# Kernel optimization log

Hardware: AMD Instinct MI355X
Metric: run time of the kernel (lower is better)

The kernel has to match this reference:

```python
import jax, jax.numpy as jnp
import numpy as np

N = 100000
E = 1600000
IN, HID, OUT = 128, 256, 128


def setup_inputs() -> dict:
    key = jax.random.key(0)
    ks = jax.random.split(key, 8)
    x = jax.random.normal(ks[0], (N, IN), dtype=jnp.float32)
    edge_index = jax.random.randint(ks[1], (2, E), 0, N, dtype=jnp.int64)
    # PyG SAGEConv params: lin_l (neighbor aggr, with bias), lin_r (root, no bias)
    def glorot(k, shape):
        fan_in = shape[1]
        return jax.random.normal(k, shape, dtype=jnp.float32) / jnp.sqrt(jnp.float32(fan_in))
    W1l = glorot(ks[2], (HID, IN)); b1 = jnp.zeros((HID,), jnp.float32)
    W1r = glorot(ks[3], (HID, IN))
    W2l = glorot(ks[4], (OUT, HID)); b2 = jnp.zeros((OUT,), jnp.float32)
    W2r = glorot(ks[5], (OUT, HID))
    return {"x": x, "edge_index": edge_index, "W1l": W1l, "b1": b1,
            "W1r": W1r, "W2l": W2l, "b2": b2, "W2r": W2r}


def sage_conv(x, row, col, Wl, b, Wr, n_nodes):
    # mean-aggregate neighbor features x[row] at target nodes col
    msg = x[row]                                               # [E, d]
    s = jax.ops.segment_sum(msg, col, num_segments=n_nodes)    # [N, d]
    deg = jax.ops.segment_sum(jnp.ones((row.shape[0], 1), x.dtype), col,
                              num_segments=n_nodes)            # [N, 1]
    mean = s / jnp.maximum(deg, 1.0)
    return mean @ Wl.T + b + x @ Wr.T


def reference(x, edge_index, W1l, b1, W1r, W2l, b2, W2r):
    row, col = edge_index[0], edge_index[1]
    h = sage_conv(x, row, col, W1l, b1, W1r, N)
    h = jax.nn.relu(h)
    # dropout is identity in eval mode
    out = sage_conv(h, row, col, W2l, b2, W2r, N)
    return out
```

## Files before the change

### kernel.cpp

```cpp
#include <hip/hip_runtime.h>
#include <hip/hip_bf16.h>
#include <hip/hip_fp16.h>

#define NN 100000
#define NE 1600000
#define NCHUNK ((NN + 127) / 128)
#define NPB 512
#define NB 256
#define CHUNK 8192
#define NCH ((NE + CHUNK - 1) / CHUNK)

typedef __attribute__((ext_vector_type(8))) short short8;
typedef __attribute__((ext_vector_type(4))) float float4v;
typedef __attribute__((ext_vector_type(2))) float float2v;

__device__ __forceinline__ unsigned short f2bf(float f) {
    unsigned int b = __float_as_uint(f);
    return (unsigned short)((b + 0x7fffu + ((b >> 16) & 1u)) >> 16);
}
__device__ __forceinline__ unsigned int pack_bf16(float lo, float hi) {
    return (unsigned int)f2bf(lo) | ((unsigned int)f2bf(hi) << 16);
}
__device__ __forceinline__ void addp8(float* a, uint2 u) {
    float2v f;
    f = __builtin_amdgcn_cvt_pk_f32_fp8(u.x, false); a[0] += f.x; a[1] += f.y;
    f = __builtin_amdgcn_cvt_pk_f32_fp8(u.x, true);  a[2] += f.x; a[3] += f.y;
    f = __builtin_amdgcn_cvt_pk_f32_fp8(u.y, false); a[4] += f.x; a[5] += f.y;
    f = __builtin_amdgcn_cvt_pk_f32_fp8(u.y, true);  a[6] += f.x; a[7] += f.y;
}
__device__ __forceinline__ unsigned char f2fp8(float v) {
    int r = __builtin_amdgcn_cvt_pk_fp8_f32(v, v, 0, false);
    return (unsigned char)(r & 0xff);
}
__device__ __forceinline__ unsigned short pack2fp8(float lo, float hi) {
    int r = __builtin_amdgcn_cvt_pk_fp8_f32(lo, hi, 0, false);
    return (unsigned short)(r & 0xffff);
}
__device__ __forceinline__ float h2f(unsigned short u) {
    return __half2float(__ushort_as_half(u));
}

__global__ void k_prep(const float* x, const float* W1l, const float* W1r,
                       const float* W2l, const float* W2r, const int* ei,
                       unsigned int* axb_u, unsigned short* xf8, unsigned short* wb1,
                       unsigned short* wb2, int* bcnt) {
    __shared__ int hh[NB];
    int b = blockIdx.x, t = threadIdx.x;
    if (b < 3125) {
#pragma unroll
        for (int k = 0; k < 8; k++) {
            int tt = b * 2048 + k * 256 + t;
            int node = tt >> 6, i = tt & 63;
            float2 v = ((const float2*)x)[tt];
            axb_u[(size_t)node * 128 + 64 + i] = pack_bf16(v.x, v.y);
            xf8[(size_t)node * 64 + i] = pack2fp8(v.x, v.y);
        }
    } else if (b < 3253) {
        int i = (b - 3125) * 256 + t;
        int r1 = i >> 7, c1 = i & 127;
        wb1[r1 * 256 + c1]       = f2bf(W1l[i]);
        wb1[r1 * 256 + 128 + c1] = f2bf(W1r[i]);
        wb2[i]         = f2bf(W2l[i]);
        wb2[32768 + i] = f2bf(W2r[i]);
    } else {
        hh[t] = 0;
        __syncthreads();
        int e0 = (b - 3253) * 6250;
        for (int e = e0 + t; e < e0 + 6250; e += 256)
            atomicAdd(&hh[ei[NE + e] >> 9], 1);
        __syncthreads();
        if (hh[t]) atomicAdd(&bcnt[t], hh[t]);
    }
}

__global__ void k_bscan(const int* bcnt, int* boff, int* bcur) {
    __shared__ int s[NB];
    int t = threadIdx.x;
    int v = bcnt[t];
    s[t] = v;
    __syncthreads();
    for (int d = 1; d < NB; d <<= 1) {
        int val = (t >= d) ? s[t - d] : 0;
        __syncthreads();
        s[t] += val;
        __syncthreads();
    }
    boff[t + 1] = s[t];
    if (t == 0) boff[0] = 0;
    bcur[t] = s[t] - v;
}

__global__ __launch_bounds__(256) void k_bscatter(const int* ei, int* bcur, unsigned int* pairs) {
    __shared__ unsigned int buf[CHUNK];
    __shared__ int cnt[NB];
    __shared__ int lbase[NB];
    __shared__ int lcur[NB];
    __shared__ int gpos[NB];
    int t = threadIdx.x;
    int e0 = blockIdx.x * CHUNK;
    int nedge = NE - e0; if (nedge > CHUNK) nedge = CHUNK;
    cnt[t] = 0;
    __syncthreads();
    for (int i = t; i < nedge; i += 256)
        atomicAdd(&cnt[ei[NE + e0 + i] >> 9], 1);
    __syncthreads();
    int v = cnt[t];
    lcur[t] = v;
    __syncthreads();
    for (int d = 1; d < NB; d <<= 1) {
        int val = (t >= d) ? lcur[t - d] : 0;
        __syncthreads();
        lcur[t] += val;
        __syncthreads();
    }
    lbase[t] = lcur[t] - v;
    gpos[t] = atomicAdd(&bcur[t], v);
    __syncthreads();
    lcur[t] = lbase[t];
    __syncthreads();
    for (int i = t; i < nedge; i += 256) {
        int r = ei[e0 + i], c = ei[NE + e0 + i];
        int b = c >> 9;
        int p = atomicAdd(&lcur[b], 1);
        buf[p] = (unsigned)r | ((unsigned)(c & 511) << 17);
    }
    __syncthreads();
    int wv = t >> 6, lane = t & 63;
    for (int b = wv; b < NB; b += 4) {
        int n = cnt[b], lb = lbase[b], gp = gpos[b];
        for (int i = lane; i < n; i += 64)
            pairs[gp + i] = buf[lb + i];
    }
}

__global__ __launch_bounds__(256) void k_build(const unsigned int* pairs, const int* boff,
                                               int* off, int* deg, int* csr, int* csr16) {
    __shared__ int ldeg[NPB];
    __shared__ int lcur[NPB];
    __shared__ int lini[NPB];
    __shared__ int sscan[256];
    int b = blockIdx.x;
    int nbase = b * NPB;
    if (nbase >= NN) return;
    int t = threadIdx.x;
    int base = boff[b], cntb = boff[b + 1] - base;
    ldeg[t] = 0; ldeg[t + 256] = 0;
    __syncthreads();
    for (int i = t; i < cntb; i += 256) {
        unsigned int pr = pairs[base + i];
        atomicAdd(&ldeg[pr >> 17], 1);
    }
    __syncthreads();
    int d0 = ldeg[2 * t], d1 = ldeg[2 * t + 1];
    int v = d0 + d1;
    sscan[t] = v;
    __syncthreads();
    for (int d = 1; d < 256; d <<= 1) {
        int val = (t >= d) ? sscan[t - d] : 0;
        __syncthreads();
        sscan[t] += val;
        __syncthreads();
    }
    int ex = sscan[t] - v;
    lcur[2 * t] = ex;      lcur[2 * t + 1] = ex + d0;
    lini[2 * t] = ex;      lini[2 * t + 1] = ex + d0;
    __syncthreads();
    int nloc = NN - nbase; if (nloc > NPB) nloc = NPB;
    for (int ln = t; ln < nloc; ln += 256) {
        off[nbase + ln] = base + lcur[ln];
        deg[nbase + ln] = ldeg[ln];
    }
    __syncthreads();
    if (csr16) {
        for (int i = t; i < cntb; i += 256) {
            unsigned int pr = pairs[base + i];
            int nd = pr >> 17;
            int p = atomicAdd(&lcur[nd], 1);
            int src = (int)(pr & 0x1FFFFu);
            csr[base + p] = src;
            int rk = p - lini[nd];
            if (rk < 16) csr16[(size_t)(nbase + nd) * 16 + rk] = src;
        }
    } else {
        for (int i = t; i < cntb; i += 256) {
            unsigned int pr = pairs[base + i];
            int p = atomicAdd(&lcur[pr >> 17], 1);
            csr[base + p] = (int)(pr & 0x1FFFFu);
        }
    }
}

__global__ __launch_bounds__(512) void k_agg1(const uint2* xf8, const int* off, const int* deg,
                                              const int* csr, const int* csr16,
                                              unsigned int* axb_w) {
    int wid = (blockIdx.x * 512 + threadIdx.x) >> 6;
    if (wid >= NN) return;
    int lane = threadIdx.x & 63;
    int sub = lane >> 4, l16 = lane & 15;
    int start = off[wid], d = deg[wid];
    const uint2* gp = xf8 + l16;
    uint2 z; z.x = 0u; z.y = 0u;
    float a[8] = {0.f, 0.f, 0.f, 0.f, 0.f, 0.f, 0.f, 0.f};
    int j;
    if (csr16) {
        int e16 = csr16[(size_t)wid * 16 + l16];
#pragma unroll
        for (int r = 0; r < 4; r++) {
            int rk = (r << 2) | sub;
            int idx = __shfl(e16, rk, 64);
            uint2 u = (rk < d) ? gp[(size_t)idx * 16] : z;
            addp8(a, u);
        }
        j = 16 + sub;
    } else {
        j = sub;
    }
    for (; j + 4 < d; j += 8) {
        int n0 = csr[start + j];
        int n1 = csr[start + j + 4];
        uint2 u0 = gp[(size_t)n0 * 16];
        uint2 u1 = gp[(size_t)n1 * 16];
        addp8(a, u0); addp8(a, u1);
    }
    if (j < d) {
        int nb = csr[start + j];
        uint2 u = gp[(size_t)nb * 16];
        addp8(a, u);
    }
#pragma unroll
    for (int i = 0; i < 8; i++) {
        a[i] += __shfl_xor(a[i], 16, 64);
        a[i] += __shfl_xor(a[i], 32, 64);
    }
    if (sub == 0) {
        float inv = 1.0f / (float)(d > 0 ? d : 1);
        uint4 o;
        o.x = pack_bf16(a[0] * inv, a[1] * inv);
        o.y = pack_bf16(a[2] * inv, a[3] * inv);
        o.z = pack_bf16(a[4] * inv, a[5] * inv);
        o.w = pack_bf16(a[6] * inv, a[7] * inv);
        *(uint4*)(axb_w + (size_t)wid * 128 + (l16 << 2)) = o;
    }
}

__global__ __launch_bounds__(512) void k_agg2(const uint2* g, const int* off, const int* deg,
                                              const int* csr, const int* csr16,
                                              const unsigned short* partial, float* out) {
    int wid = (blockIdx.x * 512 + threadIdx.x) >> 6;
    if (wid >= NN) return;
    int lane = threadIdx.x & 63;
    int sub = lane >> 4, l16 = lane & 15;
    int start = off[wid], d = deg[wid];
    const uint2* gp = g + l16;
    uint2 z; z.x = 0u; z.y = 0u;
    uint4 pu;
    if (sub == 0)
        pu = *(const uint4*)(partial + (size_t)wid * 128 + (l16 << 3));
    float a[8] = {0.f, 0.f, 0.f, 0.f, 0.f, 0.f, 0.f, 0.f};
    int j;
    if (csr16) {
        int e16 = csr16[(size_t)wid * 16 + l16];
#pragma unroll
        for (int r = 0; r < 4; r++) {
            int rk = (r << 2) | sub;
            int idx = __shfl(e16, rk, 64);
            uint2 u = (rk < d) ? gp[(size_t)idx * 16] : z;
            addp8(a, u);
        }
        j = 16 + sub;
    } else {
        j = sub;
    }
    for (; j + 4 < d; j += 8) {
        int n0 = csr[start + j];
        int n1 = csr[start + j + 4];
        uint2 u0 = gp[(size_t)n0 * 16];
        uint2 u1 = gp[(size_t)n1 * 16];
        addp8(a, u0); addp8(a, u1);
    }
    if (j < d) {
        int nb = csr[start + j];
        uint2 u = gp[(size_t)nb * 16];
        addp8(a, u);
    }
#pragma unroll
    for (int i = 0; i < 8; i++) {
        a[i] += __shfl_xor(a[i], 16, 64);
        a[i] += __shfl_xor(a[i], 32, 64);
    }
    if (sub == 0) {
        float inv = 1.0f / (float)(d > 0 ? d : 1);
        float4 c0, c1;
        c0.x = h2f(pu.x & 0xffff) + a[0] * inv; c0.y = h2f(pu.x >> 16) + a[1] * inv;
        c0.z = h2f(pu.y & 0xffff) + a[2] * inv; c0.w = h2f(pu.y >> 16) + a[3] * inv;
        c1.x = h2f(pu.z & 0xffff) + a[4] * inv; c1.y = h2f(pu.z >> 16) + a[5] * inv;
        c1.z = h2f(pu.w & 0xffff) + a[6] * inv; c1.w = h2f(pu.w >> 16) + a[7] * inv;
        float4* po = (float4*)(out + (size_t)wid * 128) + (l16 << 1);
        po[0] = c0; po[1] = c1;
    }
}

#define BROW 264
#define GGRID (32 * ((NCHUNK + 7) / 8))
__global__ __launch_bounds__(256, 4) void k_gemm1(const unsigned short* A, const unsigned short* wb,
                                                  const float* b1, unsigned short* H) {
    __shared__ unsigned short Bs[64 * BROW];
    int t = threadIdx.x;
    int b = blockIdx.x;
    int chunk = (b & 7) + ((b >> 5) << 3);
    int cg = (b >> 3) & 3;
    if (chunk >= NCHUNK) return;
    {
        const short8* src = (const short8*)(wb + (size_t)cg * 64 * 256);
        short8* dst = (short8*)Bs;
#pragma unroll
        for (int i = 0; i < 8; i++) {
            int gi = i * 256 + t;
            int r = gi >> 5, c = gi & 31;
            dst[r * 33 + c] = src[gi];
        }
    }
    __syncthreads();
    int wv = t >> 6, lane = t & 63;
    int mrow = lane & 15, quad = lane >> 4;
    int base = chunk * 128 + wv * 32;
    if (base >= NN) return;
    float bias[4];
#pragma unroll
    for (int ctl = 0; ctl < 4; ctl++) bias[ctl] = b1[cg * 64 + ctl * 16 + mrow];
    float4v acc[2][4];
#pragma unroll
    for (int h = 0; h < 2; h++)
#pragma unroll
        for (int ctl = 0; ctl < 4; ctl++) acc[h][ctl] = (float4v)(0.0f);
    const short8* a0p = (const short8*)(A + (size_t)(base + mrow) * 256);
    const short8* a1p = (const short8*)(A + (size_t)(base + 16 + mrow) * 256);
#pragma unroll
    for (int kk = 0; kk < 8; kk++) {
        short8 a0 = a0p[kk * 4 + quad];
        short8 a1 = a1p[kk * 4 + quad];
        int koff = kk * 32 + quad * 8;
#pragma unroll
        for (int ctl = 0; ctl < 4; ctl++) {
            short8 bfr = *(const short8*)(Bs + (ctl * 16 + mrow) * BROW + koff);
            acc[0][ctl] = __builtin_amdgcn_mfma_f32_16x16x32_bf16(a0, bfr, acc[0][ctl], 0, 0, 0);
            acc[1][ctl] = __builtin_amdgcn_mfma_f32_16x16x32_bf16(a1, bfr, acc[1][ctl], 0, 0, 0);
        }
    }
#pragma unroll
    for (int ctl = 0; ctl < 4; ctl++) {
        int col = cg * 64 + ctl * 16 + mrow;
#pragma unroll
        for (int h = 0; h < 2; h++)
#pragma unroll
            for (int r = 0; r < 4; r++) {
                int node = base + h * 16 + quad * 4 + r;
                float v = acc[h][ctl][r] + bias[ctl];
                H[(size_t)node * 256 + col] = f2bf(fmaxf(v, 0.f));
            }
    }
}

__global__ __launch_bounds__(256, 4) void k_gemm2(const unsigned short* A, const unsigned short* wb,
                                                  const float* b2, unsigned char* g,
                                                  unsigned short* partial) {
    __shared__ unsigned short Bs[64 * BROW];
    int t = threadIdx.x;
    int b = blockIdx.x;
    int chunk = (b & 7) + ((b >> 5) << 3);
    int cg = (b >> 3) & 3;
    if (chunk >= NCHUNK) return;
    {
        const short8* src = (const short8*)(wb + (size_t)cg * 64 * 256);
        short8* dst = (short8*)Bs;
#pragma unroll
        for (int i = 0; i < 8; i++) {
            int gi = i * 256 + t;
            int r = gi >> 5, c = gi & 31;
            dst[r * 33 + c] = src[gi];
        }
    }
    __syncthreads();
    int wv = t >> 6, lane = t & 63;
    int mrow = lane & 15, quad = lane >> 4;
    int base = chunk * 128 + wv * 32;
    if (base >= NN) return;
    float bias[4];
#pragma unroll
    for (int ctl = 0; ctl < 4; ctl++)
        bias[ctl] = (cg >= 2) ? b2[cg * 64 + ctl * 16 + mrow - 128] : 0.f;
    float4v acc[2][4];
#pragma unroll
    for (int h = 0; h < 2; h++)
#pragma unroll
        for (int ctl = 0; ctl < 4; ctl++) acc[h][ctl] = (float4v)(0.0f);
    const short8* a0p = (const short8*)(A + (size_t)(base + mrow) * 256);
    const short8* a1p = (const short8*)(A + (size_t)(base + 16 + mrow) * 256);
#pragma unroll
    for (int kk = 0; kk < 8; kk++) {
        short8 a0 = a0p[kk * 4 + quad];
        short8 a1 = a1p[kk * 4 + quad];
        int koff = kk * 32 + quad * 8;
#pragma unroll
        for (int ctl = 0; ctl < 4; ctl++) {
            short8 bfr = *(const short8*)(Bs + (ctl * 16 + mrow) * BROW + koff);
            acc[0][ctl] = __builtin_amdgcn_mfma_f32_16x16x32_bf16(a0, bfr, acc[0][ctl], 0, 0, 0);
            acc[1][ctl] = __builtin_amdgcn_mfma_f32_16x16x32_bf16(a1, bfr, acc[1][ctl], 0, 0, 0);
        }
    }
    if (cg < 2) {
#pragma unroll
        for (int ctl = 0; ctl < 4; ctl++) {
            int col = cg * 64 + ctl * 16 + mrow;
#pragma unroll
            for (int h = 0; h < 2; h++)
#pragma unroll
                for (int r = 0; r < 4; r++) {
                    int node = base + h * 16 + quad * 4 + r;
                    g[(size_t)node * 128 + col] = f2fp8(acc[h][ctl][r]);
                }
        }
    } else {
#pragma unroll
        for (int ctl = 0; ctl < 4; ctl++) {
            int pcol = cg * 64 + ctl * 16 + mrow - 128;
#pragma unroll
            for (int h = 0; h < 2; h++)
#pragma unroll
                for (int r = 0; r < 4; r++) {
                    int node = base + h * 16 + quad * 4 + r;
                    __half hf = __float2half(acc[h][ctl][r] + bias[ctl]);
                    partial[(size_t)node * 128 + pcol] = __half_as_ushort(hf);
                }
        }
    }
}

extern "C" void kernel_launch(void* const* d_in, const int* in_sizes, int n_in,
                              void* d_out, int out_size, void* d_ws, size_t ws_size,
                              hipStream_t stream) {
    const float* x   = (const float*)d_in[0];
    const int*   ei  = (const int*)d_in[1];
    const float* W1l = (const float*)d_in[2];
    const float* b1  = (const float*)d_in[3];
    const float* W1r = (const float*)d_in[4];
    const float* W2l = (const float*)d_in[5];
    const float* b2  = (const float*)d_in[6];
    const float* W2r = (const float*)d_in[7];
    float* out = (float*)d_out;

    char* p = (char*)d_ws;
    unsigned int* axb = (unsigned int*)p; p += (size_t)NN * 256 * 2;
    unsigned short* h = (unsigned short*)p; p += (size_t)NN * 256 * 2;
    unsigned char* g  = (unsigned char*)p; p += (size_t)NN * 128;
    unsigned short* xf8 = (unsigned short*)p; p += (size_t)NN * 128;
    unsigned short* wb1 = (unsigned short*)p; p += 65536 * 2;
    unsigned short* wb2 = (unsigned short*)p; p += 65536 * 2;
    int* deg  = (int*)p; p += (size_t)NN * 4;
    int* off  = (int*)p; p += (size_t)NN * 4;
    int* csr  = (int*)p; p += (size_t)NE * 4;
    int* bcnt = (int*)p; p += NB * 4;
    int* boff = (int*)p; p += (NB + 1) * 4;
    int* bcur = (int*)p; p += NB * 4;
    if (ws_size < (size_t)(p - (char*)d_ws)) return;
    int* csr16 = (int*)p; p += (size_t)NN * 16 * 4;
    if (ws_size < (size_t)(p - (char*)d_ws)) csr16 = nullptr;
    unsigned int* pairs = (unsigned int*)h;
    unsigned short* partial = (unsigned short*)axb;

    hipMemsetAsync(bcnt, 0, NB * 4, stream);
    k_prep<<<3509, 256, 0, stream>>>(x, W1l, W1r, W2l, W2r, ei, axb, xf8, wb1, wb2, bcnt);
    k_bscan<<<1, NB, 0, stream>>>(bcnt, boff, bcur);
    k_bscatter<<<NCH, 256, 0, stream>>>(ei, bcur, pairs);
    k_build<<<NB, 256, 0, stream>>>(pairs, boff, off, deg, csr, csr16);
    k_agg1<<<12500, 512, 0, stream>>>((const uint2*)xf8, off, deg, csr, csr16, axb);
    k_gemm1<<<GGRID, 256, 0, stream>>>((const unsigned short*)axb, wb1, b1, h);
    k_gemm2<<<GGRID, 256, 0, stream>>>(h, wb2, b2, g, partial);
    k_agg2<<<12500, 512, 0, stream>>>((const uint2*)g, off, deg, csr, csr16, partial, out);
}
```

Before: 356.1 us.

## Restructure aggregation to full-wave per-neighbor gathers with 32-slot padded CSR and zero row

Both aggregation kernels now have each lane own two features, and the whole wave walks neighbors one at a time. This replaces the 4-way sub-wave split and its cross-lane shuffle reduction. The padded per-node neighbor table grows from 16 to 32 slots, and the first 32 neighbors are gathered in a fully unrolled loop. Padding slots point at a zeroed sentinel row N, which k_prep now writes in an extra block, so the loop needs no per-load predicate. This trades 2-byte loads per lane and wasted loads for low-degree nodes (mean degree 16) against more memory-level parallelism and no reduction; the padded table also doubles in size.

```diff
diff --git a/kernel.cpp b/kernel.cpp
--- a/kernel.cpp
+++ b/kernel.cpp
@@ -21,13 +21,6 @@
 __device__ __forceinline__ unsigned int pack_bf16(float lo, float hi) {
     return (unsigned int)f2bf(lo) | ((unsigned int)f2bf(hi) << 16);
 }
-__device__ __forceinline__ void addp8(float* a, uint2 u) {
-    float2v f;
-    f = __builtin_amdgcn_cvt_pk_f32_fp8(u.x, false); a[0] += f.x; a[1] += f.y;
-    f = __builtin_amdgcn_cvt_pk_f32_fp8(u.x, true);  a[2] += f.x; a[3] += f.y;
-    f = __builtin_amdgcn_cvt_pk_f32_fp8(u.y, false); a[4] += f.x; a[5] += f.y;
-    f = __builtin_amdgcn_cvt_pk_f32_fp8(u.y, true);  a[6] += f.x; a[7] += f.y;
-}
 __device__ __forceinline__ unsigned char f2fp8(float v) {
     int r = __builtin_amdgcn_cvt_pk_fp8_f32(v, v, 0, false);
     return (unsigned char)(r & 0xff);
@@ -43,7 +36,7 @@
 __global__ void k_prep(const float* x, const float* W1l, const float* W1r,
                        const float* W2l, const float* W2r, const int* ei,
                        unsigned int* axb_u, unsigned short* xf8, unsigned short* wb1,
-                       unsigned short* wb2, int* bcnt) {
+                       unsigned short* wb2, int* bcnt, unsigned short* gz) {
     __shared__ int hh[NB];
     int b = blockIdx.x, t = threadIdx.x;
     if (b < 3125) {
@@ -62,7 +55,7 @@
         wb1[r1 * 256 + 128 + c1] = f2bf(W1r[i]);
         wb2[i]         = f2bf(W2l[i]);
         wb2[32768 + i] = f2bf(W2r[i]);
-    } else {
+    } else if (b < 3509) {
         hh[t] = 0;
         __syncthreads();
         int e0 = (b - 3253) * 6250;
@@ -70,6 +63,9 @@
             atomicAdd(&hh[ei[NE + e] >> 9], 1);
         __syncthreads();
         if (hh[t]) atomicAdd(&bcnt[t], hh[t]);
+    } else {
+        if (t < 64) xf8[(size_t)NN * 64 + t] = 0;
+        else if (t < 128 && gz) gz[(size_t)NN * 64 + (t - 64)] = 0;
     }
 }
 
@@ -134,7 +130,7 @@
 }
 
 __global__ __launch_bounds__(256) void k_build(const unsigned int* pairs, const int* boff,
-                                               int* off, int* deg, int* csr, int* csr16) {
+                                               int* off, int* deg, int* csr, int* csr32) {
     __shared__ int ldeg[NPB];
     __shared__ int lcur[NPB];
     __shared__ int lini[NPB];
@@ -171,7 +167,7 @@
         deg[nbase + ln] = ldeg[ln];
     }
     __syncthreads();
-    if (csr16) {
+    if (csr32) {
         for (int i = t; i < cntb; i += 256) {
             unsigned int pr = pairs[base + i];
             int nd = pr >> 17;
@@ -179,7 +175,7 @@
             int src = (int)(pr & 0x1FFFFu);
             csr[base + p] = src;
             int rk = p - lini[nd];
-            if (rk < 16) csr16[(size_t)(nbase + nd) * 16 + rk] = src;
+            if (rk < 32) csr32[(size_t)(nbase + nd) * 32 + rk] = src;
         }
     } else {
         for (int i = t; i < cntb; i += 256) {
@@ -190,114 +186,90 @@
     }
 }
 
-__global__ __launch_bounds__(512) void k_agg1(const uint2* xf8, const int* off, const int* deg,
-                                              const int* csr, const int* csr16,
+__global__ __launch_bounds__(512) void k_agg1(const unsigned short* xf8, const int* off,
+                                              const int* deg, const int* csr, const int* csr32,
                                               unsigned int* axb_w) {
     int wid = (blockIdx.x * 512 + threadIdx.x) >> 6;
     if (wid >= NN) return;
+    int widu = __builtin_amdgcn_readfirstlane(wid);
     int lane = threadIdx.x & 63;
-    int sub = lane >> 4, l16 = lane & 15;
-    int start = off[wid], d = deg[wid];
-    const uint2* gp = xf8 + l16;
-    uint2 z; z.x = 0u; z.y = 0u;
-    float a[8] = {0.f, 0.f, 0.f, 0.f, 0.f, 0.f, 0.f, 0.f};
-    int j;
-    if (csr16) {
-        int e16 = csr16[(size_t)wid * 16 + l16];
-#pragma unroll
-        for (int r = 0; r < 4; r++) {
-            int rk = (r << 2) | sub;
-            int idx = __shfl(e16, rk, 64);
-            uint2 u = (rk < d) ? gp[(size_t)idx * 16] : z;
-            addp8(a, u);
-        }
-        j = 16 + sub;
+    int d = deg[widu];
+    float a0 = 0.f, a1 = 0.f;
+    if (csr32) {
+        const int* c32 = csr32 + (size_t)widu * 32;
+        int dm = d < 32 ? d : 32;
+#pragma unroll
+        for (int r = 0; r < 32; r++) {
+            int idx = (r < dm) ? c32[r] : NN;
+            unsigned short u = xf8[(size_t)idx * 64 + lane];
+            float2v f = __builtin_amdgcn_cvt_pk_f32_fp8((unsigned int)u, false);
+            a0 += f.x; a1 += f.y;
+        }
+        if (d > 32) {
+            int start = off[widu];
+            for (int j = 32; j < d; j++) {
+                int idx = csr[start + j];
+                unsigned short u = xf8[(size_t)idx * 64 + lane];
+                float2v f = __builtin_amdgcn_cvt_pk_f32_fp8((unsigned int)u, false);
+                a0 += f.x; a1 += f.y;
+            }
+        }
     } else {
-        j = sub;
-    }
-    for (; j + 4 < d; j += 8) {
-        int n0 = csr[start + j];
-        int n1 = csr[start + j + 4];
-        uint2 u0 = gp[(size_t)n0 * 16];
-        uint2 u1 = gp[(size_t)n1 * 16];
-        addp8(a, u0); addp8(a, u1);
-    }
-    if (j < d) {
-        int nb = csr[start + j];
-        uint2 u = gp[(size_t)nb * 16];
-        addp8(a, u);
-    }
-#pragma unroll
-    for (int i = 0; i < 8; i++) {
-        a[i] += __shfl_xor(a[i], 16, 64);
-        a[i] += __shfl_xor(a[i], 32, 64);
-    }
-    if (sub == 0) {
-        float inv = 1.0f / (float)(d > 0 ? d : 1);
-        uint4 o;
-        o.x = pack_bf16(a[0] * inv, a[1] * inv);
-        o.y = pack_bf16(a[2] * inv, a[3] * inv);
-        o.z = pack_bf16(a[4] * inv, a[5] * inv);
-        o.w = pack_bf16(a[6] * inv, a[7] * inv);
-        *(uint4*)(axb_w + (size_t)wid * 128 + (l16 << 2)) = o;
-    }
-}
-
-__global__ __launch_bounds__(512) void k_agg2(const uint2* g, const int* off, const int* deg,
-                                              const int* csr, const int* csr16,
+        int start = off[widu];
+        for (int j = 0; j < d; j++) {
+            int idx = csr[start + j];
+            unsigned short u = xf8[(size_t)idx * 64 + lane];
+            float2v f = __builtin_amdgcn_cvt_pk_f32_fp8((unsigned int)u, false);
+            a0 += f.x; a1 += f.y;
+        }
+    }
+    float inv = 1.0f / (float)(d > 0 ? d : 1);
+    axb_w[(size_t)wid * 128 + lane] = pack_bf16(a0 * inv, a1 * inv);
+}
+
+__global__ __launch_bounds__(512) void k_agg2(const unsigned short* g, const int* off,
+                                              const int* deg, const int* csr, const int* csr32,
                                               const unsigned short* partial, float* out) {
     int wid = (blockIdx.x * 512 + threadIdx.x) >> 6;
     if (wid >= NN) return;
+    int widu = __builtin_amdgcn_readfirstlane(wid);
     int lane = threadIdx.x & 63;
-    int sub = lane >> 4, l16 = lane & 15;
-    int start = off[wid], d = deg[wid];
-    const uint2* gp = g + l16;
-    uint2 z; z.x = 0u; z.y = 0u;
-    uint4 pu;
-    if (sub == 0)
-        pu = *(const uint4*)(partial + (size_t)wid * 128 + (l16 << 3));
-    float a[8] = {0.f, 0.f, 0.f, 0.f, 0.f, 0.f, 0.f, 0.f};
-    int j;
-    if (csr16) {
-        int e16 = csr16[(size_t)wid * 16 + l16];
-#pragma unroll
-        for (int r = 0; r < 4; r++) {
-            int rk = (r << 2) | sub;
-            int idx = __shfl(e16, rk, 64);
-            uint2 u = (rk < d) ? gp[(size_t)idx * 16] : z;
-            addp8(a, u);
-        }
-        j = 16 + sub;
+    int d = deg[widu];
+    unsigned int pu = *(const unsigned int*)(partial + (size_t)widu * 128 + (lane << 1));
+    float a0 = 0.f, a1 = 0.f;
+    if (csr32) {
+        const int* c32 = csr32 + (size_t)widu * 32;
+        int dm = d < 32 ? d : 32;
+#pragma unroll
+        for (int r = 0; r < 32; r++) {
+            int idx = (r < dm) ? c32[r] : NN;
+            unsigned short u = g[(size_t)idx * 64 + lane];
+            float2v f = __builtin_amdgcn_cvt_pk_f32_fp8((unsigned int)u, false);
+            a0 += f.x; a1 += f.y;
+        }
+        if (d > 32) {
+            int start = off[widu];
+            for (int j = 32; j < d; j++) {
+                int idx = csr[start + j];
+                unsigned short u = g[(size_t)idx * 64 + lane];
+                float2v f = __builtin_amdgcn_cvt_pk_f32_fp8((unsigned int)u, false);
+                a0 += f.x; a1 += f.y;
+            }
+        }
     } else {
-        j = sub;
-    }
-    for (; j + 4 < d; j += 8) {
-        int n0 = csr[start + j];
-        int n1 = csr[start + j + 4];
-        uint2 u0 = gp[(size_t)n0 * 16];
-        uint2 u1 = gp[(size_t)n1 * 16];
-        addp8(a, u0); addp8(a, u1);
-    }
-    if (j < d) {
-        int nb = csr[start + j];
-        uint2 u = gp[(size_t)nb * 16];
-        addp8(a, u);
-    }
-#pragma unroll
-    for (int i = 0; i < 8; i++) {
-        a[i] += __shfl_xor(a[i], 16, 64);
-        a[i] += __shfl_xor(a[i], 32, 64);
-    }
-    if (sub == 0) {
-        float inv = 1.0f / (float)(d > 0 ? d : 1);
-        float4 c0, c1;
-        c0.x = h2f(pu.x & 0xffff) + a[0] * inv; c0.y = h2f(pu.x >> 16) + a[1] * inv;
-        c0.z = h2f(pu.y & 0xffff) + a[2] * inv; c0.w = h2f(pu.y >> 16) + a[3] * inv;
-        c1.x = h2f(pu.z & 0xffff) + a[4] * inv; c1.y = h2f(pu.z >> 16) + a[5] * inv;
-        c1.z = h2f(pu.w & 0xffff) + a[6] * inv; c1.w = h2f(pu.w >> 16) + a[7] * inv;
-        float4* po = (float4*)(out + (size_t)wid * 128) + (l16 << 1);
-        po[0] = c0; po[1] = c1;
-    }
+        int start = off[widu];
+        for (int j = 0; j < d; j++) {
+            int idx = csr[start + j];
+            unsigned short u = g[(size_t)idx * 64 + lane];
+            float2v f = __builtin_amdgcn_cvt_pk_f32_fp8((unsigned int)u, false);
+            a0 += f.x; a1 += f.y;
+        }
+    }
+    float inv = 1.0f / (float)(d > 0 ? d : 1);
+    float2 o;
+    o.x = h2f((unsigned short)(pu & 0xffff)) + a0 * inv;
+    o.y = h2f((unsigned short)(pu >> 16)) + a1 * inv;
+    *(float2*)(out + (size_t)wid * 128 + (lane << 1)) = o;
 }
 
 #define BROW 264
@@ -452,8 +424,8 @@
     char* p = (char*)d_ws;
     unsigned int* axb = (unsigned int*)p; p += (size_t)NN * 256 * 2;
     unsigned short* h = (unsigned short*)p; p += (size_t)NN * 256 * 2;
-    unsigned char* g  = (unsigned char*)p; p += (size_t)NN * 128;
-    unsigned short* xf8 = (unsigned short*)p; p += (size_t)NN * 128;
+    unsigned char* g  = (unsigned char*)p; p += (size_t)NN * 128 + 256;
+    unsigned short* xf8 = (unsigned short*)p; p += (size_t)NN * 128 + 256;
     unsigned short* wb1 = (unsigned short*)p; p += 65536 * 2;
     unsigned short* wb2 = (unsigned short*)p; p += 65536 * 2;
     int* deg  = (int*)p; p += (size_t)NN * 4;
@@ -463,18 +435,19 @@
     int* boff = (int*)p; p += (NB + 1) * 4;
     int* bcur = (int*)p; p += NB * 4;
     if (ws_size < (size_t)(p - (char*)d_ws)) return;
-    int* csr16 = (int*)p; p += (size_t)NN * 16 * 4;
-    if (ws_size < (size_t)(p - (char*)d_ws)) csr16 = nullptr;
+    int* csr32 = (int*)p; p += (size_t)NN * 32 * 4;
+    if (ws_size < (size_t)(p - (char*)d_ws)) csr32 = nullptr;
     unsigned int* pairs = (unsigned int*)h;
     unsigned short* partial = (unsigned short*)axb;
 
     hipMemsetAsync(bcnt, 0, NB * 4, stream);
-    k_prep<<<3509, 256, 0, stream>>>(x, W1l, W1r, W2l, W2r, ei, axb, xf8, wb1, wb2, bcnt);
+    k_prep<<<3510, 256, 0, stream>>>(x, W1l, W1r, W2l, W2r, ei, axb, xf8, wb1, wb2, bcnt,
+                                     (unsigned short*)g);
     k_bscan<<<1, NB, 0, stream>>>(bcnt, boff, bcur);
     k_bscatter<<<NCH, 256, 0, stream>>>(ei, bcur, pairs);
-    k_build<<<NB, 256, 0, stream>>>(pairs, boff, off, deg, csr, csr16);
-    k_agg1<<<12500, 512, 0, stream>>>((const uint2*)xf8, off, deg, csr, csr16, axb);
+    k_build<<<NB, 256, 0, stream>>>(pairs, boff, off, deg, csr, csr32);
+    k_agg1<<<12500, 512, 0, stream>>>(xf8, off, deg, csr, csr32, axb);
     k_gemm1<<<GGRID, 256, 0, stream>>>((const unsigned short*)axb, wb1, b1, h);
     k_gemm2<<<GGRID, 256, 0, stream>>>(h, wb2, b2, g, partial);
-    k_agg2<<<12500, 512, 0, stream>>>((const uint2*)g, off, deg, csr, csr16, partial, out);
-}
+    k_agg2<<<12500, 512, 0, stream>>>((const unsigned short*)g, off, deg, csr, csr32, partial, out);
+}
```

New measurement: 362.3 us. Within noise of the previous version (+1.7%).
